# Performance work log

Hardware: AMD Instinct MI355X
Metric: run time of the kernel (lower is better)

Reference implementation:

```python
import jax, jax.numpy as jnp
import numpy as np

D, H, DH, L, DFF, V, K = 512, 8, 64, 6, 2048, 256, 5
N = 10240
TAU = 0.1
EPS = 1e-5


def _ln(x, w, b):
    m = x.mean(-1, keepdims=True)
    v = ((x - m) ** 2).mean(-1, keepdims=True)
    return (x - m) * jax.lax.rsqrt(v + EPS) * w + b


def _attn(q_in, kv_in, inw, inb, ow, ob):
    # q_in: [Q, D], kv_in: [M, D]; standard PyTorch MultiheadAttention math
    wq, wk, wv = jnp.split(inw, 3, 0)
    bq, bk, bv = jnp.split(inb, 3)
    q = (q_in @ wq.T + bq).reshape(-1, H, DH)
    k = (kv_in @ wk.T + bk).reshape(-1, H, DH)
    v = (kv_in @ wv.T + bv).reshape(-1, H, DH)
    s = jnp.einsum('qhd,mhd->hqm', q, k) / np.float32(np.sqrt(DH))
    o = jnp.einsum('hqm,mhd->qhd', jax.nn.softmax(s, -1), v).reshape(-1, D)
    return o @ ow.T + ob


def setup_inputs() -> dict:
    key = jax.random.key(0)
    ks = iter(jax.random.split(key, 64))

    def w(shape):
        return jax.random.normal(next(ks), shape, jnp.float32) * 0.02

    inp = {
        'input_bytes': jax.random.randint(next(ks), (N,), 0, V, jnp.int32),
        'emb': w((V, D)),
        'alpha': jnp.float32(0.5),
        'enc_inw': w((L, 3 * D, D)), 'enc_inb': w((L, 3 * D)),
        'enc_ow': w((L, D, D)), 'enc_ob': w((L, D)),
        'enc_w1': w((L, DFF, D)), 'enc_b1': w((L, DFF)),
        'enc_w2': w((L, D, DFF)), 'enc_b2': w((L, D)),
        'enc_ln1w': jnp.ones((L, D)), 'enc_ln1b': jnp.zeros((L, D)),
        'enc_ln2w': jnp.ones((L, D)), 'enc_ln2b': jnp.zeros((L, D)),
        'dec_sa_inw': w((L, 3 * D, D)), 'dec_sa_inb': w((L, 3 * D)),
        'dec_sa_ow': w((L, D, D)), 'dec_sa_ob': w((L, D)),
        'dec_ca_inw': w((L, 3 * D, D)), 'dec_ca_inb': w((L, 3 * D)),
        'dec_ca_ow': w((L, D, D)), 'dec_ca_ob': w((L, D)),
        'dec_w1': w((L, DFF, D)), 'dec_b1': w((L, DFF)),
        'dec_w2': w((L, D, DFF)), 'dec_b2': w((L, D)),
        'dec_ln1w': jnp.ones((L, D)), 'dec_ln1b': jnp.zeros((L, D)),
        'dec_ln2w': jnp.ones((L, D)), 'dec_ln2b': jnp.zeros((L, D)),
        'dec_ln3w': jnp.ones((L, D)), 'dec_ln3b': jnp.zeros((L, D)),
        'out_w': w((V, D)), 'out_b': w((V,)),
    }
    return inp


def reference(input_bytes, emb, alpha, enc_inw, enc_inb, enc_ow, enc_ob,
              enc_w1, enc_b1, enc_w2, enc_b2, enc_ln1w, enc_ln1b, enc_ln2w, enc_ln2b,
              dec_sa_inw, dec_sa_inb, dec_sa_ow, dec_sa_ob,
              dec_ca_inw, dec_ca_inb, dec_ca_ow, dec_ca_ob,
              dec_w1, dec_b1, dec_w2, dec_b2,
              dec_ln1w, dec_ln1b, dec_ln2w, dec_ln2b, dec_ln3w, dec_ln3b,
              out_w, out_b):
    P = input_bytes.shape[0] // K
    patches = input_bytes[:P * K].reshape(P, K)            # fixed k-byte patching
    x = emb[patches].mean(1)                               # mean-pooled patch embeddings [P, D]
    # ---- TransformerEncoder (post-LN, relu FFN, no dropout at eval) ----
    for l in range(L):
        x = _ln(x + _attn(x, x, enc_inw[l], enc_inb[l], enc_ow[l], enc_ob[l]), enc_ln1w[l], enc_ln1b[l])
        ff = jax.nn.relu(x @ enc_w1[l].T + enc_b1[l]) @ enc_w2[l].T + enc_b2[l]
        x = _ln(x + ff, enc_ln2w[l], enc_ln2b[l])
    encoded = x                                            # [P, D]
    # ---- gating + embedding mix (vectorized over the per-patch loop) ----
    gate = jnp.linalg.norm(encoded, axis=-1) > TAU
    tok = emb[patches[:, -1]]
    x = jnp.where(gate[:, None], alpha * encoded + (1.0 - alpha) * tok, tok)  # [P, D]
    # ---- TransformerDecoder: each patch is an independent length-1 target;
    #      self-attn over a single token reduces to out_proj(V(x));
    #      cross-attn attends to the full encoded memory (as in the original loop) ----
    for l in range(L):
        wv = dec_sa_inw[l][2 * D:]
        bv = dec_sa_inb[l][2 * D:]
        sa = (x @ wv.T + bv) @ dec_sa_ow[l].T + dec_sa_ob[l]
        x = _ln(x + sa, dec_ln1w[l], dec_ln1b[l])
        ca = _attn(x, encoded, dec_ca_inw[l], dec_ca_inb[l], dec_ca_ow[l], dec_ca_ob[l])
        x = _ln(x + ca, dec_ln2w[l], dec_ln2b[l])
        ff = jax.nn.relu(x @ dec_w1[l].T + dec_b1[l]) @ dec_w2[l].T + dec_b2[l]
        x = _ln(x + ff, dec_ln3w[l], dec_ln3b[l])
    return x @ out_w.T + out_b                             # [P, V]
```

## Files before the change

### kernel.cpp

```cpp
#include <hip/hip_runtime.h>
#include <hip/hip_bf16.h>
#include <math.h>

#define DD   512
#define HN   8
#define DHD  64
#define LL   6
#define DFF_ 2048
#define VV   256
#define KB_  5
#define PP   2048
#define EPS_ 1e-5f
#define TAU_ 0.1f
#define NS   4
#define KVS  (PP / NS)

typedef __attribute__((ext_vector_type(8))) short bf16x8;
typedef __attribute__((ext_vector_type(4))) short bf16x4;
typedef __attribute__((ext_vector_type(4))) float f32x4;

__device__ __forceinline__ float wave_sum(float v) {
#pragma unroll
  for (int m = 32; m >= 1; m >>= 1) v += __shfl_xor(v, m, 64);
  return v;
}

__device__ __forceinline__ unsigned short f2bf(float f) {
  unsigned u = __float_as_uint(f);
  u += 0x7FFF + ((u >> 16) & 1);
  return (unsigned short)(u >> 16);
}

__device__ __forceinline__ bf16x8 cvt8(float4 a, float4 b) {
  bf16x8 v;
  v[0] = (short)f2bf(a.x); v[1] = (short)f2bf(a.y);
  v[2] = (short)f2bf(a.z); v[3] = (short)f2bf(a.w);
  v[4] = (short)f2bf(b.x); v[5] = (short)f2bf(b.y);
  v[6] = (short)f2bf(b.z); v[7] = (short)f2bf(b.w);
  return v;
}

__device__ __forceinline__ void gload16(const void* g, void* l) {
  __builtin_amdgcn_global_load_lds(
      (const __attribute__((address_space(1))) unsigned int*)g,
      (__attribute__((address_space(3))) unsigned int*)l, 16, 0, 0);
}

#define NSEG 55
struct CvtSeg { const float* src; short* dst; int n; };
struct CvtArgs { CvtSeg seg[NSEG]; };

__global__ __launch_bounds__(256) void convert_bf16_kernel(CvtArgs a) {
  const CvtSeg sg = a.seg[blockIdx.y];
  const int i = ((int)blockIdx.x * 256 + (int)threadIdx.x) * 8;
  if (i >= sg.n) return;
  const float4 x0 = *(const float4*)(sg.src + i);
  const float4 x1 = *(const float4*)(sg.src + i + 4);
  *(bf16x8*)(sg.dst + i) = cvt8(x0, x1);
}

__global__ __launch_bounds__(256) void transpose_wv_kernel(const float* __restrict__ sa_inw,
                                                           short* __restrict__ wvt) {
  __shared__ float t[64][65];
  const int l = blockIdx.z;
  const float* S = sa_inw + (size_t)l * 3 * DD * DD + (size_t)2 * DD * DD;
  short* D = wvt + (size_t)l * DD * DD;
  const int bo = blockIdx.y * 64;
  const int bi = blockIdx.x * 64;
  const int r = (int)threadIdx.x >> 2;
  const int c0 = ((int)threadIdx.x & 3) * 16;
#pragma unroll
  for (int j = 0; j < 16; j += 4)
    *(float4*)&t[r][c0 + j] = *(const float4*)&S[(size_t)(bo + r) * DD + bi + c0 + j];
  __syncthreads();
  bf16x8 o0, o1;
#pragma unroll
  for (int j = 0; j < 8; ++j) o0[j] = (short)f2bf(t[c0 + j][r]);
#pragma unroll
  for (int j = 0; j < 8; ++j) o1[j] = (short)f2bf(t[c0 + 8 + j][r]);
  short* dp = &D[(size_t)(bi + r) * DD + bo + c0];
  *(bf16x8*)dp = o0;
  *(bf16x8*)(dp + 8) = o1;
}

__global__ __launch_bounds__(256) void sa_bias_kernel(const float* __restrict__ sa_inb,
                                                      const float* __restrict__ sa_ow,
                                                      const float* __restrict__ sa_ob,
                                                      float* __restrict__ bc) {
  const int gid = (int)blockIdx.x * 4 + ((int)threadIdx.x >> 6);
  const int l = gid >> 9, n = gid & 511;
  const int lane = (int)threadIdx.x & 63;
  const float* wo = sa_ow + (size_t)l * DD * DD + (size_t)n * DD + lane * 8;
  const float* bv = sa_inb + (size_t)l * 3 * DD + 2 * DD + lane * 8;
  float s = 0.f;
#pragma unroll
  for (int j = 0; j < 8; ++j) s += wo[j] * bv[j];
  s = wave_sum(s);
  if (lane == 0) bc[(size_t)l * DD + n] = s + sa_ob[(size_t)l * DD + n];
}

__global__ __launch_bounds__(256) void gemm_wc_kernel(const short* __restrict__ WoBase,
                                                      size_t astr,
                                                      const short* __restrict__ WvT,
                                                      short* __restrict__ Wc) {
  constexpr int BK = 64;
  __shared__ short As[64 * BK];
  __shared__ short Bs[64 * BK];
  const int l = blockIdx.z;
  const short* A = WoBase + (size_t)l * astr;
  const short* W = WvT + (size_t)l * DD * DD;
  short* C = Wc + (size_t)l * DD * DD;
  const int tid = (int)threadIdx.x;
  const int lane = tid & 63;
  const int wid = tid >> 6;
  const int wm = (wid >> 1) * 32;
  const int wn = (wid & 1) * 32;
  const int bm = blockIdx.y * 64;
  const int bn = blockIdx.x * 64;
  const int fr = lane & 15;
  const int kq = lane >> 4;
  const int rs = fr & 7;
  const int srow = lane >> 3;
  const int scg = (lane & 7) ^ srow;

  f32x4 acc[2][2];
#pragma unroll
  for (int i = 0; i < 2; ++i)
#pragma unroll
    for (int j = 0; j < 2; ++j) acc[i][j] = (f32x4){0.f, 0.f, 0.f, 0.f};

  for (int k0 = 0; k0 < DD; k0 += BK) {
    __syncthreads();
#pragma unroll
    for (int is = 0; is < 2; ++is) {
      const int ib = is * 4 + wid;
      gload16(&A[(size_t)(bm + ib * 8 + srow) * DD + k0 + scg * 8], &As[ib * 512]);
      gload16(&W[(size_t)(bn + ib * 8 + srow) * DD + k0 + scg * 8], &Bs[ib * 512]);
    }
    __syncthreads();
#pragma unroll
    for (int s = 0; s < 2; ++s) {
      const int cg = s * 4 + kq;
      const int co = (cg ^ rs) * 8;
      bf16x8 af[2], bf[2];
#pragma unroll
      for (int i = 0; i < 2; ++i) af[i] = *(const bf16x8*)&As[(wm + i * 16 + fr) * BK + co];
#pragma unroll
      for (int j = 0; j < 2; ++j) bf[j] = *(const bf16x8*)&Bs[(wn + j * 16 + fr) * BK + co];
#pragma unroll
      for (int i = 0; i < 2; ++i)
#pragma unroll
        for (int j = 0; j < 2; ++j)
          acc[i][j] = __builtin_amdgcn_mfma_f32_16x16x32_bf16(af[i], bf[j], acc[i][j], 0, 0, 0);
    }
  }
  const int cr = (lane >> 4) * 4;
#pragma unroll
  for (int j = 0; j < 2; ++j) {
    const int col = bn + wn + j * 16 + fr;
#pragma unroll
    for (int i = 0; i < 2; ++i)
#pragma unroll
      for (int r = 0; r < 4; ++r)
        C[(size_t)(bm + wm + i * 16 + cr + r) * DD + col] = (short)f2bf(acc[i][j][r]);
  }
}

__global__ __launch_bounds__(256) void embed_mean_kernel(const int* __restrict__ bytes,
                                                         const float* __restrict__ emb,
                                                         float* __restrict__ x,
                                                         short* __restrict__ xb,
                                                         float* __restrict__ tok) {
  const int p = blockIdx.x;
  const int d = threadIdx.x * 2;
  float a0 = 0.f, a1 = 0.f;
  int last = 0;
#pragma unroll
  for (int k = 0; k < KB_; ++k) {
    const int idx = bytes[p * KB_ + k];
    last = idx;
    const float* e = emb + (size_t)idx * DD + d;
    a0 += e[0]; a1 += e[1];
  }
  a0 *= 0.2f; a1 *= 0.2f;
  x[(size_t)p * DD + d]     = a0;
  x[(size_t)p * DD + d + 1] = a1;
  xb[(size_t)p * DD + d]     = (short)f2bf(a0);
  xb[(size_t)p * DD + d + 1] = (short)f2bf(a1);
  const float* e = emb + (size_t)last * DD + d;
  tok[(size_t)p * DD + d]     = e[0];
  tok[(size_t)p * DD + d + 1] = e[1];
}

template <int BM, int BN, int NSPLIT, int RELU, int WF32, int WBF16, int QS>
__global__ __launch_bounds__(256) void gemm_gl_kernel(
    const short* __restrict__ A, int lda,
    const short* __restrict__ W, int ldw,
    const float* __restrict__ bias,
    float* __restrict__ Cf, short* __restrict__ Cb, int ldc, int Kd,
    size_t pstride) {
  constexpr int BK = 64;
  __shared__ short As[BM * BK];
  __shared__ short Bs[BN * BK];
  constexpr int WM = BM / 2, WN = BN / 2;
  constexpr int MF = WM / 16, NF = WN / 16;
  const int tid = (int)threadIdx.x;
  const int lane = tid & 63;
  const int wid = tid >> 6;
  const int wm = (wid >> 1) * WM;
  const int wn = (wid & 1) * WN;
  const int bm = blockIdx.y * BM;
  const int bn = blockIdx.x * BN;
  const int fr = lane & 15;
  const int kq = lane >> 4;
  const int rs = fr & 7;
  const int srow = lane >> 3;
  const int scg = (lane & 7) ^ srow;

  const int kz = (NSPLIT > 1) ? (int)blockIdx.z : 0;
  const int kbeg = kz * (Kd / NSPLIT);
  const int kend = kbeg + Kd / NSPLIT;

  f32x4 acc[MF][NF];
#pragma unroll
  for (int i = 0; i < MF; ++i)
#pragma unroll
    for (int j = 0; j < NF; ++j) acc[i][j] = (f32x4){0.f, 0.f, 0.f, 0.f};

  for (int k0 = kbeg; k0 < kend; k0 += BK) {
    __syncthreads();
#pragma unroll
    for (int is = 0; is < BM / 32; ++is) {
      const int ib = is * 4 + wid;
      gload16(&A[(size_t)(bm + ib * 8 + srow) * lda + k0 + scg * 8], &As[ib * 512]);
    }
#pragma unroll
    for (int is = 0; is < BN / 32; ++is) {
      const int ib = is * 4 + wid;
      gload16(&W[(size_t)(bn + ib * 8 + srow) * ldw + k0 + scg * 8], &Bs[ib * 512]);
    }
    __syncthreads();
#pragma unroll
    for (int s = 0; s < 2; ++s) {
      const int cg = s * 4 + kq;
      const int co = (cg ^ rs) * 8;
      bf16x8 af[MF], bf[NF];
#pragma unroll
      for (int i = 0; i < MF; ++i)
        af[i] = *(const bf16x8*)&As[(wm + i * 16 + fr) * BK + co];
#pragma unroll
      for (int j = 0; j < NF; ++j)
        bf[j] = *(const bf16x8*)&Bs[(wn + j * 16 + fr) * BK + co];
#pragma unroll
      for (int i = 0; i < MF; ++i)
#pragma unroll
        for (int j = 0; j < NF; ++j)
          acc[i][j] = __builtin_amdgcn_mfma_f32_16x16x32_bf16(af[i], bf[j], acc[i][j], 0, 0, 0);
    }
  }

  const int cr = (lane >> 4) * 4;
  if constexpr (NSPLIT > 1) {
    float* dst = Cf + (size_t)kz * pstride;
#pragma unroll
    for (int j = 0; j < NF; ++j) {
      const int col = bn + wn + j * 16 + fr;
#pragma unroll
      for (int i = 0; i < MF; ++i)
#pragma unroll
        for (int r = 0; r < 4; ++r)
          dst[(size_t)(bm + wm + i * 16 + cr + r) * ldc + col] = acc[i][j][r];
    }
  } else {
#pragma unroll
    for (int j = 0; j < NF; ++j) {
      const int col = bn + wn + j * 16 + fr;
      const float bb = bias[col];
      const float sc = (QS && col < DD) ? 0.125f : 1.f;
#pragma unroll
      for (int i = 0; i < MF; ++i) {
#pragma unroll
        for (int r = 0; r < 4; ++r) {
          float v = (acc[i][j][r] + bb) * sc;
          if (RELU) v = fmaxf(v, 0.f);
          const size_t idx = (size_t)(bm + wm + i * 16 + cr + r) * ldc + col;
          if (WF32) Cf[idx] = v;
          if (WBF16) Cb[idx] = (short)f2bf(v);
        }
      }
    }
  }
}

__global__ __launch_bounds__(256) void gemm_ca_kernel(
    const short* __restrict__ Aq, const short* __restrict__ Akv,
    const short* __restrict__ Wfull, const float* __restrict__ bias,
    short* __restrict__ Cb) {
  constexpr int BK = 64;
  __shared__ short As[64 * BK];
  __shared__ short Bs[64 * BK];
  const int bx = (int)blockIdx.x;
  const int part_kv = bx >= 8;
  const short* A = part_kv ? Akv : Aq;
  const int wrow0 = part_kv ? DD + (bx - 8) * 64 : bx * 64;
  const float sc = part_kv ? 1.f : 0.125f;
  const int tid = (int)threadIdx.x;
  const int lane = tid & 63;
  const int wid = tid >> 6;
  const int wm = (wid >> 1) * 32;
  const int wn = (wid & 1) * 32;
  const int bm = blockIdx.y * 64;
  const int fr = lane & 15;
  const int kq = lane >> 4;
  const int rs = fr & 7;
  const int srow = lane >> 3;
  const int scg = (lane & 7) ^ srow;

  f32x4 acc[2][2];
#pragma unroll
  for (int i = 0; i < 2; ++i)
#pragma unroll
    for (int j = 0; j < 2; ++j) acc[i][j] = (f32x4){0.f, 0.f, 0.f, 0.f};

  for (int k0 = 0; k0 < DD; k0 += BK) {
    __syncthreads();
#pragma unroll
    for (int is = 0; is < 2; ++is) {
      const int ib = is * 4 + wid;
      gload16(&A[(size_t)(bm + ib * 8 + srow) * DD + k0 + scg * 8], &As[ib * 512]);
      gload16(&Wfull[(size_t)(wrow0 + ib * 8 + srow) * DD + k0 + scg * 8], &Bs[ib * 512]);
    }
    __syncthreads();
#pragma unroll
    for (int s = 0; s < 2; ++s) {
      const int cg = s * 4 + kq;
      const int co = (cg ^ rs) * 8;
      bf16x8 af[2], bf[2];
#pragma unroll
      for (int i = 0; i < 2; ++i) af[i] = *(const bf16x8*)&As[(wm + i * 16 + fr) * BK + co];
#pragma unroll
      for (int j = 0; j < 2; ++j) bf[j] = *(const bf16x8*)&Bs[(wn + j * 16 + fr) * BK + co];
#pragma unroll
      for (int i = 0; i < 2; ++i)
#pragma unroll
        for (int j = 0; j < 2; ++j)
          acc[i][j] = __builtin_amdgcn_mfma_f32_16x16x32_bf16(af[i], bf[j], acc[i][j], 0, 0, 0);
    }
  }
  const int cr = (lane >> 4) * 4;
#pragma unroll
  for (int j = 0; j < 2; ++j) {
    const int col = wrow0 + wn + j * 16 + fr;
    const float bb = bias[col];
#pragma unroll
    for (int i = 0; i < 2; ++i)
#pragma unroll
      for (int r = 0; r < 4; ++r)
        Cb[(size_t)(bm + wm + i * 16 + cr + r) * (3 * DD) + col] =
            (short)f2bf((acc[i][j][r] + bb) * sc);
  }
}

__global__ __launch_bounds__(256) void flash_attn_mfma_kernel(const short* __restrict__ qkvb,
                                                              float* __restrict__ Opart,
                                                              float* __restrict__ stats) {
  constexpr int LS = 72;
  __shared__ short Ks[64 * LS];
  __shared__ short Vt[64 * LS];
  __shared__ short Ps[64 * LS];
  const int h = blockIdx.y;
  const int q0 = blockIdx.x * 64;
  const int sp = blockIdx.z;
  const int tid = (int)threadIdx.x;
  const int lane = tid & 63;
  const int wid = tid >> 6;
  const int fr = lane & 15;
  const int g = lane >> 4;
  const int kg = g * 8;

  bf16x8 qf[2];
  {
    const short* src = qkvb + (size_t)(q0 + wid * 16 + fr) * (3 * DD) + h * DHD + kg;
    qf[0] = *(const bf16x8*)src;
    qf[1] = *(const bf16x8*)(src + 32);
  }

  f32x4 acc_o[4];
#pragma unroll
  for (int df = 0; df < 4; ++df) acc_o[df] = (f32x4){0.f, 0.f, 0.f, 0.f};
  float mreg = -INFINITY, lsum = 0.f;

  const int sr8 = tid >> 3;
  const int sc8 = (tid & 7) * 8;
  const int vk2 = (tid & 31) * 2;
  const int vd8 = (tid >> 5) * 8;

  for (int t = 0; t < KVS / 64; ++t) {
    const int k0 = sp * KVS + t * 64;
    __syncthreads();
    {
#pragma unroll
      for (int p = 0; p < 64; p += 32)
        *(bf16x8*)&Ks[(sr8 + p) * LS + sc8] =
            *(const bf16x8*)&qkvb[(size_t)(k0 + sr8 + p) * (3 * DD) + DD + h * DHD + sc8];
      const short* vbase = qkvb + (size_t)(k0 + vk2) * (3 * DD) + 2 * DD + h * DHD + vd8;
      const bf16x8 v0 = *(const bf16x8*)vbase;
      const bf16x8 v1 = *(const bf16x8*)(vbase + 3 * DD);
#pragma unroll
      for (int j = 0; j < 8; ++j) {
        const unsigned pk = ((unsigned)(unsigned short)v0[j]) |
                            (((unsigned)(unsigned short)v1[j]) << 16);
        *(unsigned*)&Vt[(vd8 + j) * LS + vk2] = pk;
      }
    }
    __syncthreads();

    f32x4 st[4];
#pragma unroll
    for (int nf = 0; nf < 4; ++nf) st[nf] = (f32x4){0.f, 0.f, 0.f, 0.f};
    __builtin_amdgcn_s_setprio(1);
#pragma unroll
    for (int nf = 0; nf < 4; ++nf) {
      const bf16x8 kf0 = *(const bf16x8*)&Ks[(nf * 16 + fr) * LS + kg];
      const bf16x8 kf1 = *(const bf16x8*)&Ks[(nf * 16 + fr) * LS + kg + 32];
      st[nf] = __builtin_amdgcn_mfma_f32_16x16x32_bf16(kf0, qf[0], st[nf], 0, 0, 0);
      st[nf] = __builtin_amdgcn_mfma_f32_16x16x32_bf16(kf1, qf[1], st[nf], 0, 0, 0);
    }
    __builtin_amdgcn_s_setprio(0);

    float mx = st[0][0];
#pragma unroll
    for (int nf = 0; nf < 4; ++nf)
#pragma unroll
      for (int i = 0; i < 4; ++i) mx = fmaxf(mx, st[nf][i]);
    mx = fmaxf(mx, __shfl_xor(mx, 16, 64));
    mx = fmaxf(mx, __shfl_xor(mx, 32, 64));
    const float mn = fmaxf(mreg, mx);
    const float corr = __expf(mreg - mn);
    mreg = mn;
    float pv[4][4];
    float sum = 0.f;
#pragma unroll
    for (int nf = 0; nf < 4; ++nf)
#pragma unroll
      for (int i = 0; i < 4; ++i) {
        pv[nf][i] = __expf(st[nf][i] - mn);
        sum += pv[nf][i];
      }
    sum += __shfl_xor(sum, 16, 64);
    sum += __shfl_xor(sum, 32, 64);
    lsum = lsum * corr + sum;

    float corr_acc[4];
#pragma unroll
    for (int i = 0; i < 4; ++i)
      corr_acc[i] = __shfl(corr, (lane & 48) | (g * 4 + i), 64);
#pragma unroll
    for (int df = 0; df < 4; ++df) {
      acc_o[df][0] *= corr_acc[0]; acc_o[df][1] *= corr_acc[1];
      acc_o[df][2] *= corr_acc[2]; acc_o[df][3] *= corr_acc[3];
    }

#pragma unroll
    for (int nf = 0; nf < 4; ++nf) {
      bf16x4 pw;
#pragma unroll
      for (int i = 0; i < 4; ++i) pw[i] = (short)f2bf(pv[nf][i]);
      *(bf16x4*)&Ps[(wid * 16 + fr) * LS + nf * 16 + g * 4] = pw;
    }
    asm volatile("s_waitcnt lgkmcnt(0)" ::: "memory");

    const bf16x8 pa0 = *(const bf16x8*)&Ps[(wid * 16 + fr) * LS + kg];
    const bf16x8 pa1 = *(const bf16x8*)&Ps[(wid * 16 + fr) * LS + kg + 32];
    __builtin_amdgcn_s_setprio(1);
#pragma unroll
    for (int df = 0; df < 4; ++df) {
      const bf16x8 vb0 = *(const bf16x8*)&Vt[(df * 16 + fr) * LS + kg];
      const bf16x8 vb1 = *(const bf16x8*)&Vt[(df * 16 + fr) * LS + kg + 32];
      acc_o[df] = __builtin_amdgcn_mfma_f32_16x16x32_bf16(pa0, vb0, acc_o[df], 0, 0, 0);
      acc_o[df] = __builtin_amdgcn_mfma_f32_16x16x32_bf16(pa1, vb1, acc_o[df], 0, 0, 0);
    }
    __builtin_amdgcn_s_setprio(0);
  }

  const int orow = q0 + wid * 16 + g * 4;
#pragma unroll
  for (int df = 0; df < 4; ++df)
#pragma unroll
    for (int i = 0; i < 4; ++i)
      Opart[((size_t)sp * PP + orow + i) * DD + h * DHD + df * 16 + fr] = acc_o[df][i];
  if (g == 0) {
    const size_t si = (((size_t)sp * PP + q0 + wid * 16 + fr) * HN + h) * 2;
    stats[si]     = mreg;
    stats[si + 1] = lsum;
  }
}

__global__ __launch_bounds__(256) void attn_combine_kernel(const float* __restrict__ Opart,
                                                           const float* __restrict__ stats,
                                                           short* __restrict__ outb) {
  const int row = blockIdx.x;
  const int d = (int)threadIdx.x * 2;
  const int h = d >> 6;
  float m[NS], l[NS];
  float M = -INFINITY;
#pragma unroll
  for (int s = 0; s < NS; ++s) {
    const size_t si = (((size_t)s * PP + row) * HN + h) * 2;
    m[s] = stats[si]; l[s] = stats[si + 1];
    M = fmaxf(M, m[s]);
  }
  float L = 0.f, o0 = 0.f, o1 = 0.f;
#pragma unroll
  for (int s = 0; s < NS; ++s) {
    const float e = __expf(m[s] - M);
    L += l[s] * e;
    const float* op = Opart + ((size_t)s * PP + row) * DD + d;
    o0 += op[0] * e;
    o1 += op[1] * e;
  }
  const float inv = 1.f / L;
  outb[(size_t)row * DD + d]     = (short)f2bf(o0 * inv);
  outb[(size_t)row * DD + d + 1] = (short)f2bf(o1 * inv);
}

__global__ __launch_bounds__(256) void ln_residual_kernel(const float* __restrict__ xin,
                                                          const float* __restrict__ pA,
                                                          const float* __restrict__ pB,
                                                          const float* __restrict__ gb,
                                                          const float* __restrict__ w,
                                                          const float* __restrict__ b,
                                                          float* __restrict__ out,
                                                          short* __restrict__ outb) {
  const int row = blockIdx.x * 4 + (threadIdx.x >> 6);
  const int lane = threadIdx.x & 63;
  const size_t base = (size_t)row * DD + lane * 8;
  float v[8];
  {
    const float4 a0 = *(const float4*)&xin[base];
    const float4 a1 = *(const float4*)&xin[base + 4];
    const float4 r0 = *(const float4*)&pA[base];
    const float4 r1 = *(const float4*)&pA[base + 4];
    const float4 s0 = *(const float4*)&pB[base];
    const float4 s1 = *(const float4*)&pB[base + 4];
    const float4 g0 = *(const float4*)&gb[lane * 8];
    const float4 g1 = *(const float4*)&gb[lane * 8 + 4];
    v[0] = a0.x + r0.x + s0.x + g0.x; v[1] = a0.y + r0.y + s0.y + g0.y;
    v[2] = a0.z + r0.z + s0.z + g0.z; v[3] = a0.w + r0.w + s0.w + g0.w;
    v[4] = a1.x + r1.x + s1.x + g1.x; v[5] = a1.y + r1.y + s1.y + g1.y;
    v[6] = a1.z + r1.z + s1.z + g1.z; v[7] = a1.w + r1.w + s1.w + g1.w;
  }
  float sum = 0.f;
#pragma unroll
  for (int j = 0; j < 8; ++j) sum += v[j];
  sum = wave_sum(sum);
  const float mean = sum * (1.f / DD);
  float sq = 0.f;
#pragma unroll
  for (int j = 0; j < 8; ++j) { const float dd = v[j] - mean; sq += dd * dd; }
  sq = wave_sum(sq);
  const float rstd = rsqrtf(sq * (1.f / DD) + EPS_);
  const float* wp = w + lane * 8;
  const float* bp = b + lane * 8;
  float o[8];
#pragma unroll
  for (int j = 0; j < 8; ++j) o[j] = (v[j] - mean) * rstd * wp[j] + bp[j];
  *(float4*)&out[base] = *(float4*)&o[0];
  *(float4*)&out[base + 4] = *(float4*)&o[4];
  bf16x8 ob;
#pragma unroll
  for (int j = 0; j < 8; ++j) ob[j] = (short)f2bf(o[j]);
  *(bf16x8*)&outb[base] = ob;
}

__global__ __launch_bounds__(256) void gate_mix_kernel(const float* __restrict__ tok,
                                                       const float* __restrict__ alpha_p,
                                                       float* __restrict__ x,
                                                       short* __restrict__ xb,
                                                       short* __restrict__ encb) {
  const int row = blockIdx.x * 4 + (threadIdx.x >> 6);
  const int lane = threadIdx.x & 63;
  const size_t base = (size_t)row * DD + lane * 8;
  float e[8], t[8];
  {
    const float4 a0 = *(const float4*)&x[base];
    const float4 a1 = *(const float4*)&x[base + 4];
    const float4 b0 = *(const float4*)&tok[base];
    const float4 b1 = *(const float4*)&tok[base + 4];
    e[0] = a0.x; e[1] = a0.y; e[2] = a0.z; e[3] = a0.w;
    e[4] = a1.x; e[5] = a1.y; e[6] = a1.z; e[7] = a1.w;
    t[0] = b0.x; t[1] = b0.y; t[2] = b0.z; t[3] = b0.w;
    t[4] = b1.x; t[5] = b1.y; t[6] = b1.z; t[7] = b1.w;
  }
  bf16x8 eb;
#pragma unroll
  for (int j = 0; j < 8; ++j) eb[j] = (short)f2bf(e[j]);
  *(bf16x8*)&encb[base] = eb;
  float sq = 0.f;
#pragma unroll
  for (int j = 0; j < 8; ++j) sq += e[j] * e[j];
  sq = wave_sum(sq);
  const bool gate = sq > TAU_ * TAU_;
  const float a = *alpha_p;
  float o[8];
#pragma unroll
  for (int j = 0; j < 8; ++j) o[j] = gate ? (a * e[j] + (1.f - a) * t[j]) : t[j];
  *(float4*)&x[base] = *(float4*)&o[0];
  *(float4*)&x[base + 4] = *(float4*)&o[4];
  bf16x8 ob;
#pragma unroll
  for (int j = 0; j < 8; ++j) ob[j] = (short)f2bf(o[j]);
  *(bf16x8*)&xb[base] = ob;
}

__global__ __launch_bounds__(256) void out_combine_kernel(const float* __restrict__ P0,
                                                          const float* __restrict__ P1,
                                                          const float* __restrict__ bias,
                                                          float* __restrict__ out) {
  const size_t i = ((size_t)blockIdx.x * 256 + threadIdx.x) * 4;
  const int col = (int)(i % VV);
  const float4 a = *(const float4*)&P0[i];
  const float4 b = *(const float4*)&P1[i];
  const float4 c = *(const float4*)&bias[col];
  float4 o;
  o.x = a.x + b.x + c.x; o.y = a.y + b.y + c.y;
  o.z = a.z + b.z + c.z; o.w = a.w + b.w + c.w;
  *(float4*)&out[i] = o;
}

extern "C" void kernel_launch(void* const* d_in, const int* in_sizes, int n_in,
                              void* d_out, int out_size, void* d_ws, size_t ws_size,
                              hipStream_t stream) {
  const int*   bytes    = (const int*)d_in[0];
  const float* emb      = (const float*)d_in[1];
  const float* alpha    = (const float*)d_in[2];
  const float* enc_inw  = (const float*)d_in[3];
  const float* enc_inb  = (const float*)d_in[4];
  const float* enc_ow   = (const float*)d_in[5];
  const float* enc_ob   = (const float*)d_in[6];
  const float* enc_w1   = (const float*)d_in[7];
  const float* enc_b1   = (const float*)d_in[8];
  const float* enc_w2   = (const float*)d_in[9];
  const float* enc_b2   = (const float*)d_in[10];
  const float* enc_ln1w = (const float*)d_in[11];
  const float* enc_ln1b = (const float*)d_in[12];
  const float* enc_ln2w = (const float*)d_in[13];
  const float* enc_ln2b = (const float*)d_in[14];
  const float* dec_sa_inw = (const float*)d_in[15];
  const float* dec_sa_inb = (const float*)d_in[16];
  const float* dec_sa_ow  = (const float*)d_in[17];
  const float* dec_sa_ob  = (const float*)d_in[18];
  const float* dec_ca_inw = (const float*)d_in[19];
  const float* dec_ca_inb = (const float*)d_in[20];
  const float* dec_ca_ow  = (const float*)d_in[21];
  const float* dec_ca_ob  = (const float*)d_in[22];
  const float* dec_w1   = (const float*)d_in[23];
  const float* dec_b1   = (const float*)d_in[24];
  const float* dec_w2   = (const float*)d_in[25];
  const float* dec_b2   = (const float*)d_in[26];
  const float* dec_ln1w = (const float*)d_in[27];
  const float* dec_ln1b = (const float*)d_in[28];
  const float* dec_ln2w = (const float*)d_in[29];
  const float* dec_ln2b = (const float*)d_in[30];
  const float* dec_ln3w = (const float*)d_in[31];
  const float* dec_ln3b = (const float*)d_in[32];
  const float* out_w    = (const float*)d_in[33];
  const float* out_b    = (const float*)d_in[34];

  float* fp = (float*)d_ws;
  float* x     = fp;  fp += (size_t)PP * DD;
  float* tok   = fp;  fp += (size_t)PP * DD;
  float* Opart = fp;  fp += (size_t)NS * PP * DD;
  float* stats = fp;  fp += (size_t)NS * PP * HN * 2;
  float* tmpP  = fp;  fp += (size_t)2 * PP * DD;
  float* outP  = fp;  fp += (size_t)2 * PP * VV;
  float* bcbuf = fp;  fp += (size_t)LL * DD;
  short* sp = (short*)fp;
  short* x_bf    = sp;  sp += (size_t)PP * DD;
  short* enc_bf  = sp;  sp += (size_t)PP * DD;
  short* qkv_bf  = sp;  sp += (size_t)PP * 3 * DD;
  short* attno_bf= sp;  sp += (size_t)PP * DFF_;
  short* ffh_bf  = sp;  sp += (size_t)PP * DFF_;
  short* wvT     = sp;  sp += (size_t)LL * DD * DD;
  short* wcM     = sp;  sp += (size_t)LL * DD * DD;
  short* warena  = sp;

  CvtArgs ca;
  size_t eoff[LL][4], doff[LL][5], ooff;
  size_t dec_start = 0, dec_stride = 0;
  {
    int si = 0;
    size_t off = 0;
    const size_t n0 = 3 * DD * DD, n1 = DD * DD, n2 = (size_t)DFF_ * DD, n3 = (size_t)DD * DFF_;
    for (int l = 0; l < LL; ++l) {
      ca.seg[si++] = {enc_inw + (size_t)l * n0, warena + off, (int)n0}; eoff[l][0] = off; off += n0;
      ca.seg[si++] = {enc_ow  + (size_t)l * n1, warena + off, (int)n1}; eoff[l][1] = off; off += n1;
      ca.seg[si++] = {enc_w1  + (size_t)l * n2, warena + off, (int)n2}; eoff[l][2] = off; off += n2;
      ca.seg[si++] = {enc_w2  + (size_t)l * n3, warena + off, (int)n3}; eoff[l][3] = off; off += n3;
    }
    dec_start = off;
    for (int l = 0; l < LL; ++l) {
      const size_t o0 = off;
      ca.seg[si++] = {dec_sa_ow  + (size_t)l * n1, warena + off, (int)n1}; doff[l][0] = off; off += n1;
      ca.seg[si++] = {dec_ca_inw + (size_t)l * n0, warena + off, (int)n0}; doff[l][1] = off; off += n0;
      ca.seg[si++] = {dec_ca_ow  + (size_t)l * n1, warena + off, (int)n1}; doff[l][2] = off; off += n1;
      ca.seg[si++] = {dec_w1     + (size_t)l * n2, warena + off, (int)n2}; doff[l][3] = off; off += n2;
      ca.seg[si++] = {dec_w2     + (size_t)l * n3, warena + off, (int)n3}; doff[l][4] = off; off += n3;
      if (l == 0) dec_stride = off - o0; (void)o0;
    }
    ca.seg[si++] = {out_w, warena + off, VV * DD}; ooff = off;
  }

  const dim3 b256(256);
  const dim3 gFA(PP / 64, HN, NS);
  const dim3 gQKV(3 * DD / 64, PP / 128);
  const dim3 gFF1(DFF_ / 64, PP / 128);
  const dim3 gS(DD / 64, PP / 64, 2);
  const dim3 gCA(24, PP / 64);
  const dim3 gOUTg(VV / 64, PP / 64, 2);
  const size_t psD = (size_t)PP * DD;
  const size_t psV = (size_t)PP * VV;

  convert_bf16_kernel<<<dim3(512, NSEG), b256, 0, stream>>>(ca);
  transpose_wv_kernel<<<dim3(8, 8, LL), b256, 0, stream>>>(dec_sa_inw, wvT);
  sa_bias_kernel<<<(LL * DD) / 4, b256, 0, stream>>>(dec_sa_inb, dec_sa_ow, dec_sa_ob, bcbuf);
  gemm_wc_kernel<<<dim3(8, 8, LL), b256, 0, stream>>>(warena + dec_start, dec_stride, wvT, wcM);
  embed_mean_kernel<<<PP, b256, 0, stream>>>(bytes, emb, x, x_bf, tok);

  for (int l = 0; l < LL; ++l) {
    const float* inb = enc_inb + (size_t)l * 3 * DD;
    const float* ob  = enc_ob  + (size_t)l * DD;
    const float* b1  = enc_b1  + (size_t)l * DFF_;
    const float* b2  = enc_b2  + (size_t)l * DD;

    gemm_gl_kernel<128, 64, 1, 0, 0, 1, 1><<<gQKV, b256, 0, stream>>>(
        x_bf, DD, warena + eoff[l][0], DD, inb, nullptr, qkv_bf, 3 * DD, DD, 0);
    flash_attn_mfma_kernel<<<gFA, b256, 0, stream>>>(qkv_bf, Opart, stats);
    attn_combine_kernel<<<PP, b256, 0, stream>>>(Opart, stats, attno_bf);
    gemm_gl_kernel<64, 64, 2, 0, 1, 0, 0><<<gS, b256, 0, stream>>>(
        attno_bf, DD, warena + eoff[l][1], DD, nullptr, tmpP, nullptr, DD, DD, psD);
    ln_residual_kernel<<<PP / 4, b256, 0, stream>>>(
        x, tmpP, tmpP + psD, ob, enc_ln1w + (size_t)l * DD, enc_ln1b + (size_t)l * DD, x, x_bf);
    gemm_gl_kernel<128, 64, 1, 1, 0, 1, 0><<<gFF1, b256, 0, stream>>>(
        x_bf, DD, warena + eoff[l][2], DD, b1, nullptr, ffh_bf, DFF_, DD, 0);
    gemm_gl_kernel<64, 64, 2, 0, 1, 0, 0><<<gS, b256, 0, stream>>>(
        ffh_bf, DFF_, warena + eoff[l][3], DFF_, nullptr, tmpP, nullptr, DD, DFF_, psD);
    ln_residual_kernel<<<PP / 4, b256, 0, stream>>>(
        x, tmpP, tmpP + psD, b2, enc_ln2w + (size_t)l * DD, enc_ln2b + (size_t)l * DD, x, x_bf);
  }

  gate_mix_kernel<<<PP / 4, b256, 0, stream>>>(tok, alpha, x, x_bf, enc_bf);

  for (int l = 0; l < LL; ++l) {
    const float* ca_inb = dec_ca_inb + (size_t)l * 3 * DD;
    const float* ca_ob  = dec_ca_ob + (size_t)l * DD;
    const float* b1 = dec_b1 + (size_t)l * DFF_;
    const float* b2 = dec_b2 + (size_t)l * DD;

    gemm_gl_kernel<64, 64, 2, 0, 1, 0, 0><<<gS, b256, 0, stream>>>(
        x_bf, DD, wcM + (size_t)l * DD * DD, DD, nullptr, tmpP, nullptr, DD, DD, psD);
    ln_residual_kernel<<<PP / 4, b256, 0, stream>>>(
        x, tmpP, tmpP + psD, bcbuf + (size_t)l * DD,
        dec_ln1w + (size_t)l * DD, dec_ln1b + (size_t)l * DD, x, x_bf);

    gemm_ca_kernel<<<gCA, b256, 0, stream>>>(
        x_bf, enc_bf, warena + doff[l][1], ca_inb, qkv_bf);
    flash_attn_mfma_kernel<<<gFA, b256, 0, stream>>>(qkv_bf, Opart, stats);
    attn_combine_kernel<<<PP, b256, 0, stream>>>(Opart, stats, attno_bf);
    gemm_gl_kernel<64, 64, 2, 0, 1, 0, 0><<<gS, b256, 0, stream>>>(
        attno_bf, DD, warena + doff[l][2], DD, nullptr, tmpP, nullptr, DD, DD, psD);
    ln_residual_kernel<<<PP / 4, b256, 0, stream>>>(
        x, tmpP, tmpP + psD, ca_ob, dec_ln2w + (size_t)l * DD, dec_ln2b + (size_t)l * DD, x, x_bf);

    gemm_gl_kernel<128, 64, 1, 1, 0, 1, 0><<<gFF1, b256, 0, stream>>>(
        x_bf, DD, warena + doff[l][3], DD, b1, nullptr, ffh_bf, DFF_, DD, 0);
    gemm_gl_kernel<64, 64, 2, 0, 1, 0, 0><<<gS, b256, 0, stream>>>(
        ffh_bf, DFF_, warena + doff[l][4], DFF_, nullptr, tmpP, nullptr, DD, DFF_, psD);
    ln_residual_kernel<<<PP / 4, b256, 0, stream>>>(
        x, tmpP, tmpP + psD, b2, dec_ln3w + (size_t)l * DD, dec_ln3b + (size_t)l * DD, x, x_bf);
  }

  gemm_gl_kernel<64, 64, 2, 0, 1, 0, 0><<<gOUTg, b256, 0, stream>>>(
      x_bf, DD, warena + ooff, DD, nullptr, outP, nullptr, VV, DD, psV);
  out_combine_kernel<<<(PP * VV / 4) / 256, b256, 0, stream>>>(
      outP, outP + psV, out_b, (float*)d_out);
}
```

Before: 1.110 ms.

## Store flash-attention partials in bf16, fuse final encoder LN with gating

Split-KV flash attention partial outputs are now written as bf16 instead of fp32, halving the traffic between the attention and combine kernels, at some precision cost. The final encoder LayerNorm is fused with the gate/embedding-mix kernel, removing one launch and one pass over x. The weight conversion kernel now handles 16 elements per thread with half the grid, and the attention-output buffer is resized to its real footprint.

```diff
diff --git a/kernel.cpp b/kernel.cpp
--- a/kernel.cpp
+++ b/kernel.cpp
@@ -31,6 +31,10 @@
   return (unsigned short)(u >> 16);
 }
 
+__device__ __forceinline__ float bf2f(unsigned short u) {
+  return __uint_as_float(((unsigned)u) << 16);
+}
+
 __device__ __forceinline__ bf16x8 cvt8(float4 a, float4 b) {
   bf16x8 v;
   v[0] = (short)f2bf(a.x); v[1] = (short)f2bf(a.y);
@@ -52,11 +56,14 @@
 
 __global__ __launch_bounds__(256) void convert_bf16_kernel(CvtArgs a) {
   const CvtSeg sg = a.seg[blockIdx.y];
-  const int i = ((int)blockIdx.x * 256 + (int)threadIdx.x) * 8;
+  const int i = ((int)blockIdx.x * 256 + (int)threadIdx.x) * 16;
   if (i >= sg.n) return;
   const float4 x0 = *(const float4*)(sg.src + i);
   const float4 x1 = *(const float4*)(sg.src + i + 4);
-  *(bf16x8*)(sg.dst + i) = cvt8(x0, x1);
+  const float4 x2 = *(const float4*)(sg.src + i + 8);
+  const float4 x3 = *(const float4*)(sg.src + i + 12);
+  *(bf16x8*)(sg.dst + i)     = cvt8(x0, x1);
+  *(bf16x8*)(sg.dst + i + 8) = cvt8(x2, x3);
 }
 
 __global__ __launch_bounds__(256) void transpose_wv_kernel(const float* __restrict__ sa_inw,
@@ -362,7 +369,7 @@
 }
 
 __global__ __launch_bounds__(256) void flash_attn_mfma_kernel(const short* __restrict__ qkvb,
-                                                              float* __restrict__ Opart,
+                                                              short* __restrict__ Opart,
                                                               float* __restrict__ stats) {
   constexpr int LS = 72;
   __shared__ short Ks[64 * LS];
@@ -488,7 +495,8 @@
   for (int df = 0; df < 4; ++df)
 #pragma unroll
     for (int i = 0; i < 4; ++i)
-      Opart[((size_t)sp * PP + orow + i) * DD + h * DHD + df * 16 + fr] = acc_o[df][i];
+      Opart[((size_t)sp * PP + orow + i) * DD + h * DHD + df * 16 + fr] =
+          (short)f2bf(acc_o[df][i]);
   if (g == 0) {
     const size_t si = (((size_t)sp * PP + q0 + wid * 16 + fr) * HN + h) * 2;
     stats[si]     = mreg;
@@ -496,7 +504,7 @@
   }
 }
 
-__global__ __launch_bounds__(256) void attn_combine_kernel(const float* __restrict__ Opart,
+__global__ __launch_bounds__(256) void attn_combine_kernel(const short* __restrict__ Opart,
                                                            const float* __restrict__ stats,
                                                            short* __restrict__ outb) {
   const int row = blockIdx.x;
@@ -515,9 +523,9 @@
   for (int s = 0; s < NS; ++s) {
     const float e = __expf(m[s] - M);
     L += l[s] * e;
-    const float* op = Opart + ((size_t)s * PP + row) * DD + d;
-    o0 += op[0] * e;
-    o1 += op[1] * e;
+    const unsigned pk = *(const unsigned*)&Opart[((size_t)s * PP + row) * DD + d];
+    o0 += bf2f((unsigned short)(pk & 0xFFFF)) * e;
+    o1 += bf2f((unsigned short)(pk >> 16)) * e;
   }
   const float inv = 1.f / L;
   outb[(size_t)row * DD + d]     = (short)f2bf(o0 * inv);
@@ -573,40 +581,72 @@
   *(bf16x8*)&outb[base] = ob;
 }
 
-__global__ __launch_bounds__(256) void gate_mix_kernel(const float* __restrict__ tok,
-                                                       const float* __restrict__ alpha_p,
-                                                       float* __restrict__ x,
-                                                       short* __restrict__ xb,
-                                                       short* __restrict__ encb) {
+__global__ __launch_bounds__(256) void ln_gate_kernel(const float* __restrict__ xin,
+                                                      const float* __restrict__ pA,
+                                                      const float* __restrict__ pB,
+                                                      const float* __restrict__ gb,
+                                                      const float* __restrict__ w,
+                                                      const float* __restrict__ b,
+                                                      const float* __restrict__ tok,
+                                                      const float* __restrict__ alpha_p,
+                                                      float* __restrict__ xout,
+                                                      short* __restrict__ xb,
+                                                      short* __restrict__ encb) {
   const int row = blockIdx.x * 4 + (threadIdx.x >> 6);
   const int lane = threadIdx.x & 63;
   const size_t base = (size_t)row * DD + lane * 8;
-  float e[8], t[8];
+  float v[8];
   {
-    const float4 a0 = *(const float4*)&x[base];
-    const float4 a1 = *(const float4*)&x[base + 4];
+    const float4 a0 = *(const float4*)&xin[base];
+    const float4 a1 = *(const float4*)&xin[base + 4];
+    const float4 r0 = *(const float4*)&pA[base];
+    const float4 r1 = *(const float4*)&pA[base + 4];
+    const float4 s0 = *(const float4*)&pB[base];
+    const float4 s1 = *(const float4*)&pB[base + 4];
+    const float4 g0 = *(const float4*)&gb[lane * 8];
+    const float4 g1 = *(const float4*)&gb[lane * 8 + 4];
+    v[0] = a0.x + r0.x + s0.x + g0.x; v[1] = a0.y + r0.y + s0.y + g0.y;
+    v[2] = a0.z + r0.z + s0.z + g0.z; v[3] = a0.w + r0.w + s0.w + g0.w;
+    v[4] = a1.x + r1.x + s1.x + g1.x; v[5] = a1.y + r1.y + s1.y + g1.y;
+    v[6] = a1.z + r1.z + s1.z + g1.z; v[7] = a1.w + r1.w + s1.w + g1.w;
+  }
+  float sum = 0.f;
+#pragma unroll
+  for (int j = 0; j < 8; ++j) sum += v[j];
+  sum = wave_sum(sum);
+  const float mean = sum * (1.f / DD);
+  float sq = 0.f;
+#pragma unroll
+  for (int j = 0; j < 8; ++j) { const float dd = v[j] - mean; sq += dd * dd; }
+  sq = wave_sum(sq);
+  const float rstd = rsqrtf(sq * (1.f / DD) + EPS_);
+  const float* wp = w + lane * 8;
+  const float* bp = b + lane * 8;
+  float e[8];
+#pragma unroll
+  for (int j = 0; j < 8; ++j) e[j] = (v[j] - mean) * rstd * wp[j] + bp[j];
+  bf16x8 eb;
+#pragma unroll
+  for (int j = 0; j < 8; ++j) eb[j] = (short)f2bf(e[j]);
+  *(bf16x8*)&encb[base] = eb;
+  float nsq = 0.f;
+#pragma unroll
+  for (int j = 0; j < 8; ++j) nsq += e[j] * e[j];
+  nsq = wave_sum(nsq);
+  const bool gate = nsq > TAU_ * TAU_;
+  const float a = *alpha_p;
+  float t[8];
+  {
     const float4 b0 = *(const float4*)&tok[base];
     const float4 b1 = *(const float4*)&tok[base + 4];
-    e[0] = a0.x; e[1] = a0.y; e[2] = a0.z; e[3] = a0.w;
-    e[4] = a1.x; e[5] = a1.y; e[6] = a1.z; e[7] = a1.w;
     t[0] = b0.x; t[1] = b0.y; t[2] = b0.z; t[3] = b0.w;
     t[4] = b1.x; t[5] = b1.y; t[6] = b1.z; t[7] = b1.w;
   }
-  bf16x8 eb;
-#pragma unroll
-  for (int j = 0; j < 8; ++j) eb[j] = (short)f2bf(e[j]);
-  *(bf16x8*)&encb[base] = eb;
-  float sq = 0.f;
-#pragma unroll
-  for (int j = 0; j < 8; ++j) sq += e[j] * e[j];
-  sq = wave_sum(sq);
-  const bool gate = sq > TAU_ * TAU_;
-  const float a = *alpha_p;
   float o[8];
 #pragma unroll
   for (int j = 0; j < 8; ++j) o[j] = gate ? (a * e[j] + (1.f - a) * t[j]) : t[j];
-  *(float4*)&x[base] = *(float4*)&o[0];
-  *(float4*)&x[base + 4] = *(float4*)&o[4];
+  *(float4*)&xout[base] = *(float4*)&o[0];
+  *(float4*)&xout[base + 4] = *(float4*)&o[4];
   bf16x8 ob;
 #pragma unroll
   for (int j = 0; j < 8; ++j) ob[j] = (short)f2bf(o[j]);
@@ -670,16 +710,16 @@
   float* fp = (float*)d_ws;
   float* x     = fp;  fp += (size_t)PP * DD;
   float* tok   = fp;  fp += (size_t)PP * DD;
-  float* Opart = fp;  fp += (size_t)NS * PP * DD;
   float* stats = fp;  fp += (size_t)NS * PP * HN * 2;
   float* tmpP  = fp;  fp += (size_t)2 * PP * DD;
   float* outP  = fp;  fp += (size_t)2 * PP * VV;
   float* bcbuf = fp;  fp += (size_t)LL * DD;
   short* sp = (short*)fp;
+  short* OpartB  = sp;  sp += (size_t)NS * PP * DD;
   short* x_bf    = sp;  sp += (size_t)PP * DD;
   short* enc_bf  = sp;  sp += (size_t)PP * DD;
   short* qkv_bf  = sp;  sp += (size_t)PP * 3 * DD;
-  short* attno_bf= sp;  sp += (size_t)PP * DFF_;
+  short* attno_bf= sp;  sp += (size_t)PP * DD;
   short* ffh_bf  = sp;  sp += (size_t)PP * DFF_;
   short* wvT     = sp;  sp += (size_t)LL * DD * DD;
   short* wcM     = sp;  sp += (size_t)LL * DD * DD;
@@ -721,7 +761,7 @@
   const size_t psD = (size_t)PP * DD;
   const size_t psV = (size_t)PP * VV;
 
-  convert_bf16_kernel<<<dim3(512, NSEG), b256, 0, stream>>>(ca);
+  convert_bf16_kernel<<<dim3(256, NSEG), b256, 0, stream>>>(ca);
   transpose_wv_kernel<<<dim3(8, 8, LL), b256, 0, stream>>>(dec_sa_inw, wvT);
   sa_bias_kernel<<<(LL * DD) / 4, b256, 0, stream>>>(dec_sa_inb, dec_sa_ow, dec_sa_ob, bcbuf);
   gemm_wc_kernel<<<dim3(8, 8, LL), b256, 0, stream>>>(warena + dec_start, dec_stride, wvT, wcM);
@@ -735,8 +775,8 @@
 
     gemm_gl_kernel<128, 64, 1, 0, 0, 1, 1><<<gQKV, b256, 0, stream>>>(
         x_bf, DD, warena + eoff[l][0], DD, inb, nullptr, qkv_bf, 3 * DD, DD, 0);
-    flash_attn_mfma_kernel<<<gFA, b256, 0, stream>>>(qkv_bf, Opart, stats);
-    attn_combine_kernel<<<PP, b256, 0, stream>>>(Opart, stats, attno_bf);
+    flash_attn_mfma_kernel<<<gFA, b256, 0, stream>>>(qkv_bf, OpartB, stats);
+    attn_combine_kernel<<<PP, b256, 0, stream>>>(OpartB, stats, attno_bf);
     gemm_gl_kernel<64, 64, 2, 0, 1, 0, 0><<<gS, b256, 0, stream>>>(
         attno_bf, DD, warena + eoff[l][1], DD, nullptr, tmpP, nullptr, DD, DD, psD);
     ln_residual_kernel<<<PP / 4, b256, 0, stream>>>(
@@ -745,11 +785,15 @@
         x_bf, DD, warena + eoff[l][2], DD, b1, nullptr, ffh_bf, DFF_, DD, 0);
     gemm_gl_kernel<64, 64, 2, 0, 1, 0, 0><<<gS, b256, 0, stream>>>(
         ffh_bf, DFF_, warena + eoff[l][3], DFF_, nullptr, tmpP, nullptr, DD, DFF_, psD);
-    ln_residual_kernel<<<PP / 4, b256, 0, stream>>>(
-        x, tmpP, tmpP + psD, b2, enc_ln2w + (size_t)l * DD, enc_ln2b + (size_t)l * DD, x, x_bf);
-  }
-
-  gate_mix_kernel<<<PP / 4, b256, 0, stream>>>(tok, alpha, x, x_bf, enc_bf);
+    if (l + 1 < LL) {
+      ln_residual_kernel<<<PP / 4, b256, 0, stream>>>(
+          x, tmpP, tmpP + psD, b2, enc_ln2w + (size_t)l * DD, enc_ln2b + (size_t)l * DD, x, x_bf);
+    } else {
+      ln_gate_kernel<<<PP / 4, b256, 0, stream>>>(
+          x, tmpP, tmpP + psD, b2, enc_ln2w + (size_t)l * DD, enc_ln2b + (size_t)l * DD,
+          tok, alpha, x, x_bf, enc_bf);
+    }
+  }
 
   for (int l = 0; l < LL; ++l) {
     const float* ca_inb = dec_ca_inb + (size_t)l * 3 * DD;
@@ -765,8 +809,8 @@
 
     gemm_ca_kernel<<<gCA, b256, 0, stream>>>(
         x_bf, enc_bf, warena + doff[l][1], ca_inb, qkv_bf);
-    flash_attn_mfma_kernel<<<gFA, b256, 0, stream>>>(qkv_bf, Opart, stats);
-    attn_combine_kernel<<<PP, b256, 0, stream>>>(Opart, stats, attno_bf);
+    flash_attn_mfma_kernel<<<gFA, b256, 0, stream>>>(qkv_bf, OpartB, stats);
+    attn_combine_kernel<<<PP, b256, 0, stream>>>(OpartB, stats, attno_bf);
     gemm_gl_kernel<64, 64, 2, 0, 1, 0, 0><<<gS, b256, 0, stream>>>(
         attno_bf, DD, warena + doff[l][2], DD, nullptr, tmpP, nullptr, DD, DD, psD);
     ln_residual_kernel<<<PP / 4, b256, 0, stream>>>(
```

New measurement: 1.099 ms. Within noise of the previous version (-1.0%).
